# Kernel tuning notes

Measured on AMD Instinct MI355X. Metric: run time of the kernel, lower is better.

The kernel has to match this reference:

```python
import jax, jax.numpy as jnp
import numpy as np

BS, SEQ, D, H = 2, 2048, 1024, 16
HD = D // H  # head_dim = 64


def setup_inputs() -> dict:
    key = jax.random.key(0)
    kx, kw = jax.random.split(key)
    x = jax.random.normal(kx, (BS, SEQ, D), dtype=jnp.float32)
    # qkv Linear: weight [3D, D] (xavier_normal), bias zeros
    std = float(np.sqrt(2.0 / (D + 3 * D)))
    W_qkv = jax.random.normal(kw, (3 * D, D), dtype=jnp.float32) * std
    b_qkv = jnp.zeros((3 * D,), dtype=jnp.float32)
    return {"x": x, "W_qkv": W_qkv, "b_qkv": b_qkv}


def reference(x, W_qkv, b_qkv):
    bs, seq_len, embed_dim = x.shape
    # fused QKV projection: [bs, seq, 3D]
    qkv = x @ W_qkv.T + b_qkv
    qkv = qkv.reshape(bs, seq_len, 3, H, HD)
    qkv = jnp.transpose(qkv, (2, 0, 3, 1, 4))  # [3, bs, H, seq, HD]
    Q, K, V = qkv[0], qkv[1], qkv[2]
    # past_kv is None -> total_len == seq_len, past_len == 0
    scores = jnp.einsum("bhqd,bhkd->bhqk", Q, K) / jnp.sqrt(jnp.float32(HD))
    # causal mask: True above diagonal -> -inf
    mask = jnp.triu(jnp.ones((seq_len, seq_len), dtype=bool), k=1)
    scores = jnp.where(mask[None, None, :, :], -jnp.inf, scores)
    probs = jax.nn.softmax(scores, axis=-1)
    # attn_dropout = 0.0 (eval) -> identity
    out = jnp.einsum("bhqk,bhkd->bhqd", probs, V)
    out = jnp.transpose(out, (0, 2, 1, 3)).reshape(bs, seq_len, embed_dim)
    return (out, (K, V))
```

## Files before the change

### kernel.cpp

```cpp
#include <hip/hip_runtime.h>

typedef __bf16 bf16_t;
typedef __bf16 bf16x8 __attribute__((ext_vector_type(8)));
typedef float f32x4 __attribute__((ext_vector_type(4)));
typedef unsigned long long u64;

__device__ __forceinline__ unsigned short bfbits(float f) {
  unsigned u = __float_as_uint(f);
  u += 0x7fffu + ((u >> 16) & 1u);
  return (unsigned short)(u >> 16);
}
__device__ __forceinline__ bf16_t f2bf(float f) {
  unsigned short s = bfbits(f);
  union { unsigned short s; bf16_t b; } cv; cv.s = s; return cv.b;
}

__device__ __forceinline__ void gl16(const void* g, void* l) {
  __builtin_amdgcn_global_load_lds(
      (const __attribute__((address_space(1))) void*)g,
      (__attribute__((address_space(3))) void*)l,
      16, 0, 0);
}

__global__ __launch_bounds__(256) void cvt_kernel(const float* __restrict__ x,
                                                  const float* __restrict__ Wf,
                                                  bf16_t* __restrict__ xb,
                                                  bf16_t* __restrict__ wb) {
  const int i = blockIdx.x * 256 + threadIdx.x;
  const float* src; bf16_t* dst; int j;
  if (i < 524288) { j = i; src = x; dst = xb; }
  else            { j = i - 524288; src = Wf; dst = wb; }
  const float4* s = (const float4*)src + (size_t)j * 2;
  float4 a = s[0], b = s[1];
  bf16x8 o;
  o[0] = f2bf(a.x); o[1] = f2bf(a.y); o[2] = f2bf(a.z); o[3] = f2bf(a.w);
  o[4] = f2bf(b.x); o[5] = f2bf(b.y); o[6] = f2bf(b.z); o[7] = f2bf(b.w);
  const int row = j >> 7, jr = j & 127;
  const int dstc = (row << 7) + (jr & ~3) + ((jr & 3) ^ ((row >> 1) & 3));
  *((bf16x8*)dst + dstc) = o;
}

#define GEMM_K 1024
__global__ __launch_bounds__(256) void qkv_gemm(
    const bf16_t* __restrict__ A,
    const bf16_t* __restrict__ B,
    const float* __restrict__ bias,
    float* __restrict__ Ko, float* __restrict__ Vo,
    bf16_t* __restrict__ Qb, bf16_t* __restrict__ Kb,
    bf16_t* __restrict__ Vt,
    int* __restrict__ qcnt)
{
  if (blockIdx.x == 0 && threadIdx.x == 0) *qcnt = 0;
  __shared__ bf16_t lsA[128 * 32];
  __shared__ bf16_t lsB[128 * 32];
  const int tid = threadIdx.x;
  const int lane = tid & 63;
  const int ln = lane & 15, qd = lane >> 4;
  const int wid = tid >> 6;
  const int wm = wid & 1, wn = wid >> 1;
  const int xcd = blockIdx.x & 7;
  const int j = blockIdx.x >> 3;
  const int bn = xcd * 3 + (j % 3);
  const int bm = j / 3;
  const int m0 = bm * 128, n0 = bn * 128;
  const int qs = qd ^ ((ln >> 1) & 3);

  f32x4 acc[4][4] = {};

  const int c0 = tid, c1 = tid + 256;
  const bf16_t* ga0 = A + (size_t)(m0 + (c0 >> 2)) * GEMM_K + (c0 & 3) * 8;
  const bf16_t* ga1 = A + (size_t)(m0 + (c1 >> 2)) * GEMM_K + (c1 & 3) * 8;
  const bf16_t* gb0 = B + (size_t)(n0 + (c0 >> 2)) * GEMM_K + (c0 & 3) * 8;
  const bf16_t* gb1 = B + (size_t)(n0 + (c1 >> 2)) * GEMM_K + (c1 & 3) * 8;

  for (int k0 = 0; k0 < GEMM_K; k0 += 32) {
    __syncthreads();
    gl16(ga0 + k0, &lsA[c0 * 8]);
    gl16(ga1 + k0, &lsA[c1 * 8]);
    gl16(gb0 + k0, &lsB[c0 * 8]);
    gl16(gb1 + k0, &lsB[c1 * 8]);
    __syncthreads();
    bf16x8 af[4], bf[4];
#pragma unroll
    for (int mi = 0; mi < 4; ++mi)
      af[mi] = *(const bf16x8*)&lsA[(wm * 64 + mi * 16 + ln) * 32 + qs * 8];
#pragma unroll
    for (int ni = 0; ni < 4; ++ni)
      bf[ni] = *(const bf16x8*)&lsB[(wn * 64 + ni * 16 + ln) * 32 + qs * 8];
#pragma unroll
    for (int mi = 0; mi < 4; ++mi)
#pragma unroll
      for (int ni = 0; ni < 4; ++ni)
        acc[mi][ni] = __builtin_amdgcn_mfma_f32_16x16x32_bf16(af[mi], bf[ni], acc[mi][ni], 0, 0, 0);
  }

  const int sec = n0 >> 10;
#pragma unroll
  for (int mi = 0; mi < 4; ++mi) {
#pragma unroll
    for (int ni = 0; ni < 4; ++ni) {
      const int colg = n0 + wn * 64 + ni * 16 + ln;
      const float bv = bias[colg];
      const int cc = colg & 1023, h = cc >> 6, hd = cc & 63;
      if (sec == 2) {
        unsigned u[4];
#pragma unroll
        for (int r = 0; r < 4; ++r) {
          const int mg = m0 + wm * 64 + mi * 16 + qd * 4 + r;
          const int b = mg >> 11, s = mg & 2047;
          const float val = acc[mi][ni][r] + bv;
          Vo[((size_t)((b * 16 + h) * 2048 + s)) * 64 + hd] = val;
          u[r] = __float_as_uint(val);
        }
        const int mg0 = m0 + wm * 64 + mi * 16 + qd * 4;
        const int b0 = mg0 >> 11, s0 = mg0 & 2047;
        const unsigned lo = (u[1] & 0xFFFF0000u) | (u[0] >> 16);
        const unsigned hi = (u[3] & 0xFFFF0000u) | (u[2] >> 16);
        const size_t vb = (size_t)(b0 * 16 + h) * 131072 + (size_t)(s0 >> 6) * 4096 +
                          (size_t)hd * 64 + ((((s0 >> 3) & 7) ^ (hd & 7)) << 3) + (s0 & 7);
        *(u64*)&Vt[vb] = ((u64)hi << 32) | lo;
      } else {
#pragma unroll
        for (int r = 0; r < 4; ++r) {
          const int mg = m0 + wm * 64 + mi * 16 + qd * 4 + r;
          const int b = mg >> 11, s = mg & 2047;
          const float val = acc[mi][ni][r] + bv;
          const int bhi = b * 16 + h;
          const size_t sidx = (size_t)bhi * 131072 + (size_t)(s >> 6) * 4096 +
                              (size_t)(s & 63) * 64 + (((hd >> 3) ^ (s & 7)) << 3) + (hd & 7);
          if (sec == 0) {
            Qb[sidx] = f2bf(val * 0.18033688f);
          } else {
            Ko[((size_t)(bhi * 2048 + s)) * 64 + hd] = val;
            Kb[sidx] = f2bf(val);
          }
        }
      }
    }
  }
}

__global__ __launch_bounds__(256) void attn_kernel(
    const bf16_t* __restrict__ Qb,
    const bf16_t* __restrict__ Kb,
    const bf16_t* __restrict__ Vt,
    float* __restrict__ Out,
    int* __restrict__ qcnt)
{
  __shared__ bf16_t lq[8192];
  __shared__ bf16_t lk[8192];
  __shared__ bf16_t lv[8192];
  __shared__ bf16_t lp[8192];
  __shared__ int task_sh;
  const int tid = threadIdx.x;
  const int lane = tid & 63, ln = lane & 15, qd = lane >> 4;
  const int w = tid >> 6;
  const int l7 = ln & 7;

  for (;;) {
    __syncthreads();
    if (tid == 0) task_sh = atomicAdd(qcnt, 1);
    __syncthreads();
    const int task = task_sh;
    if (task >= 512) break;
    const int it = (task < 256) ? (15 - (task >> 5)) : ((task - 256) >> 5);
    const int bh = task & 31;
    const int b = bh >> 4, h = bh & 15;

    const bf16_t* qbase = Qb + (size_t)bh * 131072 + (size_t)it * 8192;
    const bf16_t* kbase = Kb + (size_t)bh * 131072;
    const bf16_t* vbase = Vt + (size_t)bh * 131072;

#pragma unroll
    for (int i = 0; i < 4; ++i) {
      const int cc = tid + i * 256;
      gl16(qbase + cc * 8, &lq[cc * 8]);
      gl16(kbase + cc * 8, &lk[cc * 8]);
      gl16(vbase + cc * 8, &lv[cc * 8]);
    }
    __syncthreads();

    bf16x8 afq[2][2];
#pragma unroll
    for (int kk = 0; kk < 2; ++kk)
#pragma unroll
      for (int qi = 0; qi < 2; ++qi) {
        const int row = w * 32 + qi * 16 + ln;
        afq[kk][qi] = *(const bf16x8*)&lq[(row >> 6) * 4096 + (row & 63) * 64 +
                                          (((kk * 4 + qd) ^ l7) << 3)];
      }

    f32x4 oc[2][4] = {};
    float lsum[2] = {0.f, 0.f};
    const int qg = it * 128 + w * 32 + ln;

    for (int st = 0; st <= it; ++st) {
      if (st > 0) {
        __syncthreads();
#pragma unroll
        for (int i = 0; i < 4; ++i) {
          const int cc = tid + i * 256;
          gl16(kbase + (size_t)st * 8192 + cc * 8, &lk[cc * 8]);
          gl16(vbase + (size_t)st * 8192 + cc * 8, &lv[cc * 8]);
        }
        __syncthreads();
      }
      const bool diag = (st == it);

#pragma unroll
      for (int h2 = 0; h2 < 2; ++h2) {
        const int lofs = h2 * 4096;
        f32x4 sa[4][2] = {};
#pragma unroll
        for (int kk = 0; kk < 2; ++kk) {
          bf16x8 ak[4];
#pragma unroll
          for (int ki = 0; ki < 4; ++ki)
            ak[ki] = *(const bf16x8*)&lk[lofs + (ki * 16 + ln) * 64 + (((kk * 4 + qd) ^ l7) << 3)];
#pragma unroll
          for (int ki = 0; ki < 4; ++ki)
#pragma unroll
            for (int qi = 0; qi < 2; ++qi)
              sa[ki][qi] = __builtin_amdgcn_mfma_f32_16x16x32_bf16(ak[ki], afq[kk][qi], sa[ki][qi], 0, 0, 0);
        }

#pragma unroll
        for (int qi = 0; qi < 2; ++qi) {
          const int qgl = qg + qi * 16;
          const int q = w * 32 + qi * 16 + ln;
#pragma unroll
          for (int ki = 0; ki < 4; ++ki) {
            const int kb0 = (st * 2 + h2) * 64 + ki * 16 + qd * 4;
            float p0 = __builtin_amdgcn_exp2f(sa[ki][qi][0]);
            float p1 = __builtin_amdgcn_exp2f(sa[ki][qi][1]);
            float p2 = __builtin_amdgcn_exp2f(sa[ki][qi][2]);
            float p3 = __builtin_amdgcn_exp2f(sa[ki][qi][3]);
            if (diag) {
              if (kb0 + 0 > qgl) p0 = 0.f;
              if (kb0 + 1 > qgl) p1 = 0.f;
              if (kb0 + 2 > qgl) p2 = 0.f;
              if (kb0 + 3 > qgl) p3 = 0.f;
            }
            lsum[qi] += (p0 + p1) + (p2 + p3);
            const unsigned lo = (__float_as_uint(p1) & 0xFFFF0000u) | (__float_as_uint(p0) >> 16);
            const unsigned hi = (__float_as_uint(p3) & 0xFFFF0000u) | (__float_as_uint(p2) >> 16);
            const int g = (ki * 2 + (qd >> 1)) ^ l7;
            *(u64*)&lp[q * 64 + g * 8 + (qd & 1) * 4] = ((u64)hi << 32) | lo;
          }
        }

#pragma unroll
        for (int kk = 0; kk < 2; ++kk) {
          bf16x8 afp[2], bfv[4];
#pragma unroll
          for (int qi = 0; qi < 2; ++qi) {
            const int q = w * 32 + qi * 16 + ln;
            afp[qi] = *(const bf16x8*)&lp[q * 64 + (((kk * 4 + qd) ^ l7) << 3)];
          }
#pragma unroll
          for (int ni = 0; ni < 4; ++ni)
            bfv[ni] = *(const bf16x8*)&lv[lofs + (ni * 16 + ln) * 64 + (((kk * 4 + qd) ^ l7) << 3)];
#pragma unroll
          for (int qi = 0; qi < 2; ++qi)
#pragma unroll
            for (int ni = 0; ni < 4; ++ni)
              oc[qi][ni] = __builtin_amdgcn_mfma_f32_16x16x32_bf16(afp[qi], bfv[ni], oc[qi][ni], 0, 0, 0);
        }
      }
    }

    float lsq[2];
#pragma unroll
    for (int qi = 0; qi < 2; ++qi) {
      float ls = lsum[qi];
      ls += __shfl_xor(ls, 16);
      ls += __shfl_xor(ls, 32);
      lsq[qi] = ls;
    }
#pragma unroll
    for (int qi = 0; qi < 2; ++qi) {
#pragma unroll
      for (int r = 0; r < 4; ++r) {
        const float lval = __shfl(lsq[qi], qd * 4 + r);
        const float inv = 1.0f / lval;
        const int rowq = it * 128 + w * 32 + qi * 16 + qd * 4 + r;
#pragma unroll
        for (int ni = 0; ni < 4; ++ni) {
          const int colh = ni * 16 + ln;
          Out[(size_t)(b * 2048 + rowq) * 1024 + h * 64 + colh] = oc[qi][ni][r] * inv;
        }
      }
    }
  }
}

extern "C" void kernel_launch(void* const* d_in, const int* in_sizes, int n_in,
                              void* d_out, int out_size, void* d_ws, size_t ws_size,
                              hipStream_t stream) {
  const float* x = (const float*)d_in[0];
  const float* W = (const float*)d_in[1];
  const float* bq = (const float*)d_in[2];
  float* out = (float*)d_out;
  float* Ko = out + 4194304;
  float* Vo = out + 8388608;
  char* ws = (char*)d_ws;
  bf16_t* xb = (bf16_t*)ws;
  bf16_t* wb = (bf16_t*)(ws + 8388608);
  bf16_t* Qb = (bf16_t*)(ws + 14680064);
  bf16_t* Kb = (bf16_t*)(ws + 23068672);
  bf16_t* Vt = (bf16_t*)(ws + 31457280);
  int*    qcnt = (int*)(ws + 39845888);

  hipLaunchKernelGGL(cvt_kernel, dim3(3584), dim3(256), 0, stream, x, W, xb, wb);
  hipLaunchKernelGGL(qkv_gemm, dim3(768), dim3(256), 0, stream, xb, wb, bq, Ko, Vo, Qb, Kb, Vt, qcnt);
  hipLaunchKernelGGL(attn_kernel, dim3(512), dim3(256), 0, stream, Qb, Kb, Vt, out, qcnt);
}
```

Baseline: 183.2 us.

## Triple-buffer QKV GEMM shared-memory tiles to overlap global loads with MFMA

```diff
diff --git a/kernel.cpp b/kernel.cpp
--- a/kernel.cpp
+++ b/kernel.cpp
@@ -51,8 +51,8 @@
     int* __restrict__ qcnt)
 {
   if (blockIdx.x == 0 && threadIdx.x == 0) *qcnt = 0;
-  __shared__ bf16_t lsA[128 * 32];
-  __shared__ bf16_t lsB[128 * 32];
+  __shared__ bf16_t lsA[3][4096];
+  __shared__ bf16_t lsB[3][4096];
   const int tid = threadIdx.x;
   const int lane = tid & 63;
   const int ln = lane & 15, qd = lane >> 4;
@@ -73,26 +73,46 @@
   const bf16_t* gb0 = B + (size_t)(n0 + (c0 >> 2)) * GEMM_K + (c0 & 3) * 8;
   const bf16_t* gb1 = B + (size_t)(n0 + (c1 >> 2)) * GEMM_K + (c1 & 3) * 8;
 
-  for (int k0 = 0; k0 < GEMM_K; k0 += 32) {
-    __syncthreads();
-    gl16(ga0 + k0, &lsA[c0 * 8]);
-    gl16(ga1 + k0, &lsA[c1 * 8]);
-    gl16(gb0 + k0, &lsB[c0 * 8]);
-    gl16(gb1 + k0, &lsB[c1 * 8]);
-    __syncthreads();
+  auto stage = [&](int t, int slot) {
+    const int ko = t * 32;
+    gl16(ga0 + ko, &lsA[slot][c0 * 8]);
+    gl16(ga1 + ko, &lsA[slot][c1 * 8]);
+    gl16(gb0 + ko, &lsB[slot][c0 * 8]);
+    gl16(gb1 + ko, &lsB[slot][c1 * 8]);
+  };
+  auto compute = [&](int slot) {
     bf16x8 af[4], bf[4];
 #pragma unroll
     for (int mi = 0; mi < 4; ++mi)
-      af[mi] = *(const bf16x8*)&lsA[(wm * 64 + mi * 16 + ln) * 32 + qs * 8];
+      af[mi] = *(const bf16x8*)&lsA[slot][(wm * 64 + mi * 16 + ln) * 32 + qs * 8];
 #pragma unroll
     for (int ni = 0; ni < 4; ++ni)
-      bf[ni] = *(const bf16x8*)&lsB[(wn * 64 + ni * 16 + ln) * 32 + qs * 8];
+      bf[ni] = *(const bf16x8*)&lsB[slot][(wn * 64 + ni * 16 + ln) * 32 + qs * 8];
 #pragma unroll
     for (int mi = 0; mi < 4; ++mi)
 #pragma unroll
       for (int ni = 0; ni < 4; ++ni)
         acc[mi][ni] = __builtin_amdgcn_mfma_f32_16x16x32_bf16(af[mi], bf[ni], acc[mi][ni], 0, 0, 0);
+  };
+
+  stage(0, 0);
+  stage(1, 1);
+  int cur = 0, nxt = 2;
+  for (int t = 0; t < 30; ++t) {
+    asm volatile("s_waitcnt vmcnt(4)" ::: "memory");
+    __builtin_amdgcn_s_barrier();
+    stage(t + 2, nxt);
+    compute(cur);
+    cur = (cur == 2) ? 0 : cur + 1;
+    nxt = (nxt == 2) ? 0 : nxt + 1;
   }
+  asm volatile("s_waitcnt vmcnt(4)" ::: "memory");
+  __builtin_amdgcn_s_barrier();
+  compute(cur);
+  cur = (cur == 2) ? 0 : cur + 1;
+  asm volatile("s_waitcnt vmcnt(0)" ::: "memory");
+  __builtin_amdgcn_s_barrier();
+  compute(cur);
 
   const int sec = n0 >> 10;
 #pragma unroll
```

After: 172.5 us. -5.8%, faster.
